# Optimization experiments

Hardware: AMD Instinct MI355X
Metric: run time of the kernel (lower is better)

The kernel has to match this reference:

```python
import jax, jax.numpy as jnp
import numpy as np

N_HEADS = 32
N_KV = 8
N_REP = N_HEADS // N_KV  # 4
HEAD_DIM = 128
DIM = 4096


def _rope(x, cos, sin, start_pos):
    # x: (B, H, T, hd); cos/sin: (max_seq, hd//2)
    T = x.shape[2]
    c = jax.lax.dynamic_slice_in_dim(cos, start_pos, T, axis=0)[None, None]  # (1,1,T,hd/2)
    s = jax.lax.dynamic_slice_in_dim(sin, start_pos, T, axis=0)[None, None]
    x1, x2 = x[..., : HEAD_DIM // 2], x[..., HEAD_DIM // 2:]
    return jnp.concatenate([x1 * c - x2 * s, x2 * c + x1 * s], axis=-1)


def setup_inputs() -> dict:
    key = jax.random.key(0)
    ks = jax.random.split(key, 7)
    B, T = 1, 2048
    sc = 0.02
    return {
        "x": jax.random.normal(ks[0], (B, T, DIM), jnp.float32),
        "cos": jax.random.normal(ks[1], (T, HEAD_DIM // 2), jnp.float32),
        "sin": jax.random.normal(ks[2], (T, HEAD_DIM // 2), jnp.float32),
        "wq": jax.random.normal(ks[3], (N_HEADS * HEAD_DIM, DIM), jnp.float32) * sc,
        "wk": jax.random.normal(ks[4], (N_KV * HEAD_DIM, DIM), jnp.float32) * sc,
        "wv": jax.random.normal(ks[5], (N_KV * HEAD_DIM, DIM), jnp.float32) * sc,
        "wo": jax.random.normal(ks[6], (DIM, DIM), jnp.float32) * sc,
        "start_pos": 0,
    }


def reference(x, cos, sin, wq, wk, wv, wo, start_pos):
    B, T, _ = x.shape
    # Projections (nn.Linear: y = x @ W^T)
    q = (x @ wq.T).reshape(B, T, N_HEADS, HEAD_DIM).transpose(0, 2, 1, 3)  # (B,Hq,T,hd)
    k = (x @ wk.T).reshape(B, T, N_KV, HEAD_DIM).transpose(0, 2, 1, 3)    # (B,Hk,T,hd)
    v = (x @ wv.T).reshape(B, T, N_KV, HEAD_DIM).transpose(0, 2, 1, 3)
    q = _rope(q, cos, sin, start_pos)
    k = _rope(k, cos, sin, start_pos)
    # GQA: group query heads per kv head instead of materializing repeat_kv
    qg = q.reshape(B, N_KV, N_REP, T, HEAD_DIM)
    scale = 1.0 / jnp.sqrt(jnp.float32(HEAD_DIM))
    scores = jnp.einsum('bgrqd,bgkd->bgrqk', qg, k) * scale  # (B,Hk,rep,T,T)
    causal = jnp.tril(jnp.ones((T, T), dtype=bool))
    scores = jnp.where(causal, scores, jnp.finfo(scores.dtype).min)
    attn = jax.nn.softmax(scores, axis=-1)
    yg = jnp.einsum('bgrqk,bgkd->bgrqd', attn, v)  # (B,Hk,rep,T,hd)
    y = yg.reshape(B, N_HEADS, T, HEAD_DIM).transpose(0, 2, 1, 3).reshape(B, T, DIM)
    return y @ wo.T
```

## Files before the change

kernel.cpp:

```cpp
#include <hip/hip_runtime.h>
#include <hip/hip_bf16.h>
#include <stdint.h>

using bf16 = __hip_bfloat16;
using bf16x8 = __attribute__((ext_vector_type(8))) short;
using f32x4  = __attribute__((ext_vector_type(4))) float;

#define AS1 __attribute__((address_space(1)))
#define AS3 __attribute__((address_space(3)))

__device__ __forceinline__ void async_ld16(const void* g, void* l) {
    __builtin_amdgcn_global_load_lds((const AS1 void*)g, (AS3 void*)l, 16, 0, 0);
}

__device__ __forceinline__ f32x4 mfma_bf16(bf16x8 a, bf16x8 b, f32x4 c) {
    return __builtin_amdgcn_mfma_f32_16x16x32_bf16(a, b, c, 0, 0, 0);
}

__device__ __forceinline__ float sexp(float x) {
    return __expf(fmaxf(x, -80.0f));
}

template<int N> __device__ __forceinline__ float dpp_max16(float x) {
    int xi = __builtin_bit_cast(int, x);
    int yi = __builtin_amdgcn_update_dpp(xi, xi, 0x110 | N, 0xf, 0xf, false);
    return fmaxf(x, __builtin_bit_cast(float, yi));
}
template<int N> __device__ __forceinline__ float dpp_add16(float x) {
    int xi = __builtin_bit_cast(int, x);
    int yi = __builtin_amdgcn_update_dpp(0, xi, 0x110 | N, 0xf, 0xf, true);
    return x + __builtin_bit_cast(float, yi);
}
__device__ __forceinline__ float bcast15(float x) {
    return __builtin_bit_cast(float,
        __builtin_amdgcn_ds_swizzle(__builtin_bit_cast(int, x), 0x01F0));
}
__device__ __forceinline__ float redmax16(float x) {
    x = dpp_max16<1>(x); x = dpp_max16<2>(x);
    x = dpp_max16<4>(x); x = dpp_max16<8>(x);
    return bcast15(x);
}
__device__ __forceinline__ float redsum16(float x) {
    x = dpp_add16<1>(x); x = dpp_add16<2>(x);
    x = dpp_add16<4>(x); x = dpp_add16<8>(x);
    return bcast15(x);
}

__device__ __forceinline__ void cvt8(const float* p, bf16* d) {
    float4 lo = *(const float4*)p;
    float4 hi = *(const float4*)(p + 4);
    bf16 t8[8] = {__float2bfloat16(lo.x), __float2bfloat16(lo.y),
                  __float2bfloat16(lo.z), __float2bfloat16(lo.w),
                  __float2bfloat16(hi.x), __float2bfloat16(hi.y),
                  __float2bfloat16(hi.z), __float2bfloat16(hi.w)};
    *(bf16x8*)d = *(const bf16x8*)t8;
}

__global__ __launch_bounds__(256) void cvt4_k(const float* __restrict__ x,  bf16* __restrict__ xb,
                                              const float* __restrict__ wq, bf16* __restrict__ wqb,
                                              const float* __restrict__ wk, bf16* __restrict__ wkb,
                                              const float* __restrict__ wv, bf16* __restrict__ wvb) {
    int stride = gridDim.x * blockDim.x;
    for (int u = blockIdx.x * blockDim.x + threadIdx.x; u < 4194304; u += stride) {
        const float* s; bf16* d; size_t off;
        if (u < 1048576)      { s = x;  d = xb;  off = (size_t)u * 8; }
        else if (u < 3145728) { s = wq; d = wqb; off = (size_t)(u - 1048576) * 8; }
        else if (u < 3670016) { s = wk; d = wkb; off = (size_t)(u - 3145728) * 8; }
        else                  { s = wv; d = wvb; off = (size_t)(u - 3670016) * 8; }
        cvt8(s + off, d + off);
    }
}

__global__ __launch_bounds__(256) void cvt_f32_bf16(const float* __restrict__ src,
                                                    bf16* __restrict__ dst, int n8) {
    int stride = gridDim.x * blockDim.x;
    for (int u = blockIdx.x * blockDim.x + threadIdx.x; u < n8; u += stride)
        cvt8(src + (size_t)u * 8, dst + (size_t)u * 8);
}

template<bool SRCF32>
__device__ __forceinline__ void stage_tile(const void* __restrict__ src,
                                           bf16* __restrict__ s,
                                           int row0, int K, int k0, int tid) {
    if constexpr (SRCF32) {
        const float* g = (const float*)src;
        #pragma unroll
        for (int i = 0; i < 2; ++i) {
            int u = tid + 256 * i;
            int row = u >> 2, c8 = (u & 3) * 8;
            cvt8(g + (size_t)(row0 + row) * K + k0 + c8, &s[row * 32 + c8]);
        }
    } else {
        const bf16* g = (const bf16*)src;
        const int wave = tid >> 6, lane = tid & 63;
        const int c0 = wave * 64 + lane;
        const int r0 = c0 >> 2, cb0 = (c0 & 3) * 16;
        const int c1 = 256 + c0;
        const int r1 = c1 >> 2, cb1 = (c1 & 3) * 16;
        async_ld16((const char*)(g + (size_t)(row0 + r0) * K + k0) + cb0,
                   (char*)s + wave * 1024);
        async_ld16((const char*)(g + (size_t)(row0 + r1) * K + k0) + cb1,
                   (char*)s + 4096 + wave * 1024);
    }
}

template<bool AF32, bool BF32, int MODE>
__global__ __launch_bounds__(256) void gemm_bt(const void* __restrict__ A,
                                               const void* __restrict__ B,
                                               void* __restrict__ C,
                                               bf16* __restrict__ Qp,
                                               bf16* __restrict__ Kp,
                                               bf16* __restrict__ Vp,
                                               int M, int N, int K) {
    __shared__ bf16 sA[128 * 32];
    __shared__ bf16 sB[128 * 32];
    const int tid  = threadIdx.x;
    const int lane = tid & 63;
    const int wave = tid >> 6;
    const int m0 = blockIdx.y * 128;
    const int n0 = blockIdx.x * 128;
    const int mrow = (wave >> 1) * 64;
    const int ncol = (wave & 1) * 64;

    f32x4 acc[4][4] = {};

    for (int k0 = 0; k0 < K; k0 += 32) {
        __syncthreads();
        stage_tile<AF32>(A, sA, m0, K, k0, tid);
        stage_tile<BF32>(B, sB, n0, K, k0, tid);
        __syncthreads();

        bf16x8 af[4], bfr[4];
        #pragma unroll
        for (int i = 0; i < 4; ++i)
            af[i] = *(const bf16x8*)&sA[(mrow + i * 16 + (lane & 15)) * 32 + (lane >> 4) * 8];
        #pragma unroll
        for (int j = 0; j < 4; ++j)
            bfr[j] = *(const bf16x8*)&sB[(ncol + j * 16 + (lane & 15)) * 32 + (lane >> 4) * 8];
        #pragma unroll
        for (int i = 0; i < 4; ++i)
            #pragma unroll
            for (int j = 0; j < 4; ++j)
                acc[i][j] = mfma_bf16(af[i], bfr[j], acc[i][j]);
    }

    #pragma unroll
    for (int i = 0; i < 4; ++i)
        #pragma unroll
        for (int j = 0; j < 4; ++j)
            #pragma unroll
            for (int r = 0; r < 4; ++r) {
                int row = m0 + mrow + i * 16 + (lane >> 4) * 4 + r;
                int col = n0 + ncol + j * 16 + (lane & 15);
                float fv = acc[i][j][r];
                if constexpr (MODE == 0) {
                    ((bf16*)C)[(size_t)row * N + col] = __float2bfloat16(fv);
                } else if constexpr (MODE == 1) {
                    ((bf16*)C)[(size_t)col * M + row] = __float2bfloat16(fv);
                } else if constexpr (MODE == 2) {
                    bf16 v = __float2bfloat16(fv);
                    if (col < 4096)      Qp[(size_t)row * 4096 + col] = v;
                    else if (col < 5120) Kp[(size_t)row * 1024 + (col - 4096)] = v;
                    else                 Vp[(size_t)(col - 5120) * 2048 + row] = v;
                } else {
                    ((float*)C)[(size_t)row * N + col] = fv;
                }
            }
}

#define VMW(N) asm volatile("s_waitcnt vmcnt(" #N ")" ::: "memory")
#define SCB    __builtin_amdgcn_sched_barrier(0)

#define TILE2(SA, SB, SA2, SB2, T2, DOST, WT) do {                                \
    bf16x8 aF0[4], bF0[4], aF1[4], bF1[4];                                        \
    _Pragma("unroll") for (int i = 0; i < 4; ++i)                                 \
        aF0[i] = *(const bf16x8*)((SA) + offA[i][0]);                             \
    _Pragma("unroll") for (int j = 0; j < 4; ++j)                                 \
        bF0[j] = *(const bf16x8*)((SB) + offB[j][0]);                             \
    SCB;                                                                          \
    _Pragma("unroll") for (int i = 0; i < 4; ++i)                                 \
        aF1[i] = *(const bf16x8*)((SA) + offA[i][1]);                             \
    _Pragma("unroll") for (int j = 0; j < 4; ++j)                                 \
        bF1[j] = *(const bf16x8*)((SB) + offB[j][1]);                             \
    SCB;                                                                          \
    if (DOST) { stgA01(SA2, T2); stgA23(SA2, T2); stgB0(SB2, T2); stgB1(SB2, T2); } \
    asm volatile("s_waitcnt lgkmcnt(8)" ::: "memory");                            \
    SCB;                                                                          \
    __builtin_amdgcn_s_setprio(1);                                                \
    _Pragma("unroll") for (int i = 0; i < 4; ++i)                                 \
      _Pragma("unroll") for (int j = 0; j < 4; ++j)                               \
        acc[i][j] = mfma_bf16(aF0[i], bF0[j], acc[i][j]);                         \
    __builtin_amdgcn_s_setprio(0);                                                \
    SCB;                                                                          \
    asm volatile("s_waitcnt lgkmcnt(0)" ::: "memory");                            \
    SCB;                                                                          \
    __builtin_amdgcn_s_setprio(1);                                                \
    _Pragma("unroll") for (int i = 0; i < 4; ++i)                                 \
      _Pragma("unroll") for (int j = 0; j < 4; ++j)                               \
        acc[i][j] = mfma_bf16(aF1[i], bF1[j], acc[i][j]);                         \
    __builtin_amdgcn_s_setprio(0);                                                \
    SCB;                                                                          \
    WT;                                                                           \
    __builtin_amdgcn_s_barrier();                                                 \
  } while (0)

template<int MODE>
__global__ __launch_bounds__(512, 1) void gemm_8p(const bf16* __restrict__ A,
                                                  const bf16* __restrict__ B,
                                                  void* __restrict__ C,
                                                  bf16* __restrict__ Qp,
                                                  bf16* __restrict__ Kp,
                                                  bf16* __restrict__ Vp,
                                                  int M, int N, int K) {
    __shared__ __align__(16) bf16 sA0[16384], sA1[16384], sA2[16384];
    __shared__ __align__(16) bf16 sB0[8192],  sB1[8192],  sB2[8192];

    const int tid  = threadIdx.x;
    const int lane = tid & 63;
    const int wave = tid >> 6;
    const int wr   = wave >> 1;
    const int wc   = wave & 1;
    const int m0 = blockIdx.y * 256;
    const int n0 = blockIdx.x * 128;
    const int NT = K >> 6;

    int offA[4][2], offB[4][2];
    {
        const int l15 = lane & 15, l4 = lane >> 4;
        #pragma unroll
        for (int i = 0; i < 4; ++i) {
            const int ra = wr * 64 + i * 16 + l15;
            const int rb = wc * 64 + i * 16 + l15;
            #pragma unroll
            for (int kh = 0; kh < 2; ++kh) {
                offA[i][kh] = ra * 64 + (((kh * 4 + l4) ^ (ra & 7)) * 8);
                offB[i][kh] = rb * 64 + (((kh * 4 + l4) ^ (rb & 7)) * 8);
            }
        }
    }

    const int rloc = tid >> 3;
    const int qsw  = (tid & 7) ^ (rloc & 7);
    const bf16* gA0 = A + (size_t)(m0 +   0 + rloc) * K + qsw * 8;
    const bf16* gA1 = A + (size_t)(m0 +  64 + rloc) * K + qsw * 8;
    const bf16* gA2 = A + (size_t)(m0 + 128 + rloc) * K + qsw * 8;
    const bf16* gA3 = A + (size_t)(m0 + 192 + rloc) * K + qsw * 8;
    const bf16* gB0 = B + (size_t)(n0 +   0 + rloc) * K + qsw * 8;
    const bf16* gB1 = B + (size_t)(n0 +  64 + rloc) * K + qsw * 8;
    const int w512 = wave * 512;

    auto stgA01 = [&](bf16* dst, int kt) __attribute__((always_inline)) {
        async_ld16(gA0 + kt * 64, dst + w512);
        async_ld16(gA1 + kt * 64, dst + 4096 + w512);
    };
    auto stgA23 = [&](bf16* dst, int kt) __attribute__((always_inline)) {
        async_ld16(gA2 + kt * 64, dst + 8192 + w512);
        async_ld16(gA3 + kt * 64, dst + 12288 + w512);
    };
    auto stgB0 = [&](bf16* dst, int kt) __attribute__((always_inline)) {
        async_ld16(gB0 + kt * 64, dst + w512);
    };
    auto stgB1 = [&](bf16* dst, int kt) __attribute__((always_inline)) {
        async_ld16(gB1 + kt * 64, dst + 4096 + w512);
    };

    f32x4 acc[4][4] = {};

    stgA01(sA0, 0); stgA23(sA0, 0); stgB0(sB0, 0); stgB1(sB0, 0);
    stgA01(sA1, 1); stgA23(sA1, 1); stgB0(sB1, 1); stgB1(sB1, 1);
    VMW(6);
    __builtin_amdgcn_s_barrier();
    asm volatile("" ::: "memory");
    SCB;

    int t = 0;
    for (; t < NT - 6; t += 3) {
        TILE2(sA0, sB0, sA2, sB2, t + 2, true, VMW(6));
        TILE2(sA1, sB1, sA0, sB0, t + 3, true, VMW(6));
        TILE2(sA2, sB2, sA1, sB1, t + 4, true, VMW(6));
    }
    TILE2(sA0, sB0, sA2, sB2, NT - 2, true,  VMW(6));
    TILE2(sA1, sB1, sA0, sB0, NT - 1, true,  VMW(6));
    TILE2(sA2, sB2, sA0, sB0, 0,      false, VMW(0));
    TILE2(sA0, sB0, sA1, sB1, 0,      false, );
    asm volatile("s_waitcnt vmcnt(0)" ::: "memory");

    #pragma unroll
    for (int i = 0; i < 4; ++i)
        #pragma unroll
        for (int j = 0; j < 4; ++j)
            #pragma unroll
            for (int r = 0; r < 4; ++r) {
                int row = m0 + wr * 64 + i * 16 + (lane >> 4) * 4 + r;
                int col = n0 + wc * 64 + j * 16 + (lane & 15);
                float fv = acc[i][j][r];
                if constexpr (MODE == 2) {
                    bf16 v = __float2bfloat16(fv);
                    if (col < 4096)      Qp[(size_t)row * 4096 + col] = v;
                    else if (col < 5120) Kp[(size_t)row * 1024 + (col - 4096)] = v;
                    else                 Vp[(size_t)(col - 5120) * 2048 + row] = v;
                } else {
                    ((float*)C)[(size_t)row * N + col] = fv;
                }
            }
}

__global__ __launch_bounds__(256) void rope_all(bf16* __restrict__ Q,
                                                bf16* __restrict__ K,
                                                const float* __restrict__ cosp,
                                                const float* __restrict__ sinp,
                                                const int* __restrict__ spp) {
    int idx = blockIdx.x * blockDim.x + threadIdx.x;
    int d = idx & 63;
    int h = (idx >> 6) % 40;
    int t = idx / (64 * 40);
    int sp = *spp;
    float c = cosp[(size_t)(t + sp) * 64 + d];
    float s = sinp[(size_t)(t + sp) * 64 + d];
    bf16* row = (h < 32) ? (Q + (size_t)t * 4096 + h * 128)
                         : (K + (size_t)t * 1024 + (h - 32) * 128);
    float x1 = __bfloat162float(row[d]);
    float x2 = __bfloat162float(row[64 + d]);
    row[d]      = __float2bfloat16(x1 * c - x2 * s);
    row[64 + d] = __float2bfloat16(x2 * c + x1 * s);
}

#define NEG_SENT (-1.0e9f)
__global__ __launch_bounds__(256) void attn_k(const bf16* __restrict__ Q,
                                              const bf16* __restrict__ K,
                                              const bf16* __restrict__ VT,
                                              bf16* __restrict__ Y) {
    constexpr int SKS = 136;
    constexpr int SVS = 72;
    __shared__ bf16 sK[64 * SKS];
    __shared__ bf16 sVT[128 * SVS];

    const int tid  = threadIdx.x;
    const int lane = tid & 63;
    const int wave = tid >> 6;
    const int qtile = 31 - (blockIdx.x >> 5);
    const int head  = blockIdx.x & 31;
    const int g     = head >> 2;
    const int qrow0 = qtile * 64 + wave * 16;
    bf16* sPw = sK + wave * 1152;

    bf16x8 qf[4];
    {
        const bf16* qbase = Q + (size_t)(qrow0 + (lane & 15)) * 4096 + head * 128;
        #pragma unroll
        for (int kk = 0; kk < 4; ++kk)
            qf[kk] = *(const bf16x8*)(qbase + kk * 32 + (lane >> 4) * 8);
    }

    float m_i[4], l_i[4];
    #pragma unroll
    for (int r = 0; r < 4; ++r) { m_i[r] = NEG_SENT; l_i[r] = 0.f; }
    f32x4 o[8] = {};
    const float scale = 0.08838834764831845f;

    for (int kt = 0; kt <= qtile; ++kt) {
        const int kt0 = kt * 64;
        __syncthreads();
        #pragma unroll
        for (int i = 0; i < 4; ++i) {
            int c = i * 256 + tid;
            {
                int row = c >> 4, ch = c & 15;
                *(uint4*)&sK[row * SKS + ch * 8] =
                    *(const uint4*)(K + (size_t)(kt0 + row) * 1024 + g * 128 + ch * 8);
            }
            {
                int row = c >> 3, ch = c & 7;
                *(uint4*)&sVT[row * SVS + ch * 8] =
                    *(const uint4*)(VT + (size_t)(g * 128 + row) * 2048 + kt0 + ch * 8);
            }
        }
        __syncthreads();

        f32x4 s[4];
        #pragma unroll
        for (int j = 0; j < 4; ++j) {
            f32x4 a = {};
            #pragma unroll
            for (int kk = 0; kk < 4; ++kk) {
                bf16x8 kfrag = *(const bf16x8*)&sK[(j * 16 + (lane & 15)) * SKS +
                                                   kk * 32 + (lane >> 4) * 8];
                a = mfma_bf16(qf[kk], kfrag, a);
            }
            s[j] = a;
        }

        #pragma unroll
        for (int j = 0; j < 4; ++j) {
            int tk = kt0 + j * 16 + (lane & 15);
            #pragma unroll
            for (int r = 0; r < 4; ++r) {
                int tq = qrow0 + (lane >> 4) * 4 + r;
                float v = s[j][r] * scale;
                s[j][r] = (tk > tq) ? NEG_SENT : v;
            }
        }

        #pragma unroll
        for (int r = 0; r < 4; ++r) {
            float mx = fmaxf(fmaxf(s[0][r], s[1][r]), fmaxf(s[2][r], s[3][r]));
            mx = redmax16(mx);
            float mn = fmaxf(m_i[r], mx);
            float alpha = sexp(m_i[r] - mn);
            m_i[r] = mn;
            float rs = 0.f;
            #pragma unroll
            for (int j = 0; j < 4; ++j) {
                float pv = sexp(s[j][r] - mn);
                s[j][r] = pv;
                rs += pv;
            }
            l_i[r] = l_i[r] * alpha + rs;
            #pragma unroll
            for (int j2 = 0; j2 < 8; ++j2) o[j2][r] *= alpha;
        }

        __syncthreads();

        #pragma unroll
        for (int j = 0; j < 4; ++j)
            #pragma unroll
            for (int r = 0; r < 4; ++r)
                sPw[((lane >> 4) * 4 + r) * SVS + j * 16 + (lane & 15)] =
                    __float2bfloat16(s[j][r]);
        __asm__ volatile("s_waitcnt lgkmcnt(0)" ::: "memory");

        #pragma unroll
        for (int kk2 = 0; kk2 < 2; ++kk2) {
            bf16x8 pf = *(const bf16x8*)&sPw[(lane & 15) * SVS + kk2 * 32 + (lane >> 4) * 8];
            #pragma unroll
            for (int j2 = 0; j2 < 8; ++j2) {
                bf16x8 vf = *(const bf16x8*)&sVT[(j2 * 16 + (lane & 15)) * SVS +
                                                 kk2 * 32 + (lane >> 4) * 8];
                o[j2] = mfma_bf16(pf, vf, o[j2]);
            }
        }
    }

    #pragma unroll
    for (int r = 0; r < 4; ++r) l_i[r] = redsum16(l_i[r]);
    #pragma unroll
    for (int j2 = 0; j2 < 8; ++j2)
        #pragma unroll
        for (int r = 0; r < 4; ++r) {
            int t   = qrow0 + (lane >> 4) * 4 + r;
            int col = head * 128 + j2 * 16 + (lane & 15);
            Y[(size_t)t * 4096 + col] = __float2bfloat16(o[j2][r] / l_i[r]);
        }
}

extern "C" void kernel_launch(void* const* d_in, const int* in_sizes, int n_in,
                              void* d_out, int out_size, void* d_ws, size_t ws_size,
                              hipStream_t stream) {
    const float* x    = (const float*)d_in[0];
    const float* cosp = (const float*)d_in[1];
    const float* sinp = (const float*)d_in[2];
    const float* wq   = (const float*)d_in[3];
    const float* wk   = (const float*)d_in[4];
    const float* wv   = (const float*)d_in[5];
    const float* wo   = (const float*)d_in[6];
    const int*   sp   = (const int*)d_in[7];
    float* out = (float*)d_out;

    char* ws = (char*)d_ws;
    bf16* Qb = (bf16*)d_out;

    const size_t NEED = 92274688;
    if (ws_size >= NEED) {
        bf16* xb   = (bf16*)(ws);
        bf16* wqkv = (bf16*)(ws + (16u << 20));
        bf16* wob  = wqkv;
        bf16* Kb   = (bf16*)(ws + (64u << 20));
        bf16* VT   = (bf16*)(ws + (68u << 20));
        bf16* Yb   = (bf16*)(ws + (72u << 20));

        cvt4_k<<<dim3(4096), 256, 0, stream>>>(x, xb, wq, wqkv,
                                               wk, wqkv + 16777216, wv, wqkv + 20971520);

        gemm_8p<2><<<dim3(48, 8), 512, 0, stream>>>(
            xb, wqkv, nullptr, Qb, Kb, VT, 2048, 6144, 4096);

        cvt_f32_bf16<<<dim3(4096), 256, 0, stream>>>(wo, wob, 2097152);

        rope_all<<<dim3(2048 * 40 * 64 / 256), 256, 0, stream>>>(Qb, Kb, cosp, sinp, sp);

        attn_k<<<dim3(1024), 256, 0, stream>>>(Qb, Kb, VT, Yb);

        gemm_8p<3><<<dim3(32, 8), 512, 0, stream>>>(
            Yb, wob, out, nullptr, nullptr, nullptr, 2048, 4096, 4096);
    } else {
        bf16* Kb = (bf16*)(ws);
        bf16* VT = (bf16*)(ws + (4u << 20));
        bf16* Yb = (bf16*)(ws + (8u << 20));

        gemm_bt<true, true, 0><<<dim3(32, 16), 256, 0, stream>>>(
            x, wq, Qb, nullptr, nullptr, nullptr, 2048, 4096, 4096);
        gemm_bt<true, true, 0><<<dim3(8, 16), 256, 0, stream>>>(
            x, wk, Kb, nullptr, nullptr, nullptr, 2048, 1024, 4096);
        gemm_bt<true, true, 1><<<dim3(8, 16), 256, 0, stream>>>(
            x, wv, VT, nullptr, nullptr, nullptr, 2048, 1024, 4096);

        rope_all<<<dim3(2048 * 40 * 64 / 256), 256, 0, stream>>>(Qb, Kb, cosp, sinp, sp);

        attn_k<<<dim3(1024), 256, 0, stream>>>(Qb, Kb, VT, Yb);

        gemm_bt<false, true, 3><<<dim3(32, 16), 256, 0, stream>>>(
            Yb, wo, out, nullptr, nullptr, nullptr, 2048, 4096, 4096);
    }
}
```

Before: 480.9 us.

## Templatize GEMM tile shape and give attention 32 query rows per wave

Makes the pipelined bf16 GEMM generic over block M, wave-column count and B fragments per wave. The QKV projection now uses a 128x192 tile on a 32x16 grid instead of 256x128 on 48x8, so more blocks cover the CUs. The attention kernel now processes 128 query rows per block, 32 per wave, so each K/V tile loaded to LDS feeds twice as many MFMAs, with a dedicated P buffer. This halves the attention grid and raises register pressure, and causal blocks now do more masked work on the diagonal.

```diff
diff --git a/kernel.cpp b/kernel.cpp
--- a/kernel.cpp
+++ b/kernel.cpp
@@ -45,6 +45,18 @@
     x = dpp_add16<4>(x); x = dpp_add16<8>(x);
     return bcast15(x);
 }
+
+template<int N> __device__ __forceinline__ void vmw() {
+    if constexpr (N == 0) asm volatile("s_waitcnt vmcnt(0)" ::: "memory");
+    else if constexpr (N == 5) asm volatile("s_waitcnt vmcnt(5)" ::: "memory");
+    else if constexpr (N == 6) asm volatile("s_waitcnt vmcnt(6)" ::: "memory");
+}
+template<int N> __device__ __forceinline__ void lgw() {
+    if constexpr (N == 0) asm volatile("s_waitcnt lgkmcnt(0)" ::: "memory");
+    else if constexpr (N == 7) asm volatile("s_waitcnt lgkmcnt(7)" ::: "memory");
+    else if constexpr (N == 8) asm volatile("s_waitcnt lgkmcnt(8)" ::: "memory");
+}
+#define SCB __builtin_amdgcn_sched_barrier(0)
 
 __device__ __forceinline__ void cvt8(const float* p, bf16* d) {
     float4 lo = *(const float4*)p;
@@ -168,131 +180,133 @@
             }
 }
 
-#define VMW(N) asm volatile("s_waitcnt vmcnt(" #N ")" ::: "memory")
-#define SCB    __builtin_amdgcn_sched_barrier(0)
-
-#define TILE2(SA, SB, SA2, SB2, T2, DOST, WT) do {                                \
-    bf16x8 aF0[4], bF0[4], aF1[4], bF1[4];                                        \
+#define KTILE(SA, SB, SA2, SB2, T2, DOST, WTN) do {                               \
+    bf16x8 aF0[4], bF0[NFr], aF1[4], bF1[NFr];                                    \
     _Pragma("unroll") for (int i = 0; i < 4; ++i)                                 \
         aF0[i] = *(const bf16x8*)((SA) + offA[i][0]);                             \
-    _Pragma("unroll") for (int j = 0; j < 4; ++j)                                 \
+    _Pragma("unroll") for (int j = 0; j < NFr; ++j)                               \
         bF0[j] = *(const bf16x8*)((SB) + offB[j][0]);                             \
     SCB;                                                                          \
     _Pragma("unroll") for (int i = 0; i < 4; ++i)                                 \
         aF1[i] = *(const bf16x8*)((SA) + offA[i][1]);                             \
-    _Pragma("unroll") for (int j = 0; j < 4; ++j)                                 \
+    _Pragma("unroll") for (int j = 0; j < NFr; ++j)                               \
         bF1[j] = *(const bf16x8*)((SB) + offB[j][1]);                             \
     SCB;                                                                          \
-    if (DOST) { stgA01(SA2, T2); stgA23(SA2, T2); stgB0(SB2, T2); stgB1(SB2, T2); } \
-    asm volatile("s_waitcnt lgkmcnt(8)" ::: "memory");                            \
+    if (DOST) { stgA(SA2, T2); stgB(SB2, T2); }                                   \
+    lgw<4 + NFr>();                                                               \
     SCB;                                                                          \
     __builtin_amdgcn_s_setprio(1);                                                \
     _Pragma("unroll") for (int i = 0; i < 4; ++i)                                 \
-      _Pragma("unroll") for (int j = 0; j < 4; ++j)                               \
+      _Pragma("unroll") for (int j = 0; j < NFr; ++j)                             \
         acc[i][j] = mfma_bf16(aF0[i], bF0[j], acc[i][j]);                         \
     __builtin_amdgcn_s_setprio(0);                                                \
     SCB;                                                                          \
-    asm volatile("s_waitcnt lgkmcnt(0)" ::: "memory");                            \
+    lgw<0>();                                                                     \
     SCB;                                                                          \
     __builtin_amdgcn_s_setprio(1);                                                \
     _Pragma("unroll") for (int i = 0; i < 4; ++i)                                 \
-      _Pragma("unroll") for (int j = 0; j < 4; ++j)                               \
+      _Pragma("unroll") for (int j = 0; j < NFr; ++j)                             \
         acc[i][j] = mfma_bf16(aF1[i], bF1[j], acc[i][j]);                         \
     __builtin_amdgcn_s_setprio(0);                                                \
     SCB;                                                                          \
-    WT;                                                                           \
+    vmw<WTN>();                                                                   \
     __builtin_amdgcn_s_barrier();                                                 \
   } while (0)
 
-template<int MODE>
-__global__ __launch_bounds__(512, 1) void gemm_8p(const bf16* __restrict__ A,
+template<int MODE, int BM, int NWC, int NFr>
+__global__ __launch_bounds__(512, 1) void gemm_kt(const bf16* __restrict__ A,
                                                   const bf16* __restrict__ B,
                                                   void* __restrict__ C,
                                                   bf16* __restrict__ Qp,
                                                   bf16* __restrict__ Kp,
                                                   bf16* __restrict__ Vp,
                                                   int M, int N, int K) {
-    __shared__ __align__(16) bf16 sA0[16384], sA1[16384], sA2[16384];
-    __shared__ __align__(16) bf16 sB0[8192],  sB1[8192],  sB2[8192];
+    constexpr int BN  = NWC * NFr * 16;
+    constexpr int IA  = BM / 64;
+    constexpr int IB  = BN / 64;
+    constexpr int IPT = IA + IB;
+
+    __shared__ __align__(16) bf16 sA0[BM * 64], sA1[BM * 64], sA2[BM * 64];
+    __shared__ __align__(16) bf16 sB0[BN * 64], sB1[BN * 64], sB2[BN * 64];
 
     const int tid  = threadIdx.x;
     const int lane = tid & 63;
     const int wave = tid >> 6;
-    const int wr   = wave >> 1;
-    const int wc   = wave & 1;
-    const int m0 = blockIdx.y * 256;
-    const int n0 = blockIdx.x * 128;
+    const int wr   = wave / NWC;
+    const int wc   = wave % NWC;
+    const int m0 = blockIdx.y * BM;
+    const int n0 = blockIdx.x * BN;
     const int NT = K >> 6;
 
-    int offA[4][2], offB[4][2];
+    int offA[4][2], offB[NFr][2];
     {
         const int l15 = lane & 15, l4 = lane >> 4;
         #pragma unroll
         for (int i = 0; i < 4; ++i) {
             const int ra = wr * 64 + i * 16 + l15;
-            const int rb = wc * 64 + i * 16 + l15;
-            #pragma unroll
-            for (int kh = 0; kh < 2; ++kh) {
+            #pragma unroll
+            for (int kh = 0; kh < 2; ++kh)
                 offA[i][kh] = ra * 64 + (((kh * 4 + l4) ^ (ra & 7)) * 8);
-                offB[i][kh] = rb * 64 + (((kh * 4 + l4) ^ (rb & 7)) * 8);
-            }
+        }
+        #pragma unroll
+        for (int j = 0; j < NFr; ++j) {
+            const int rb = wc * (NFr * 16) + j * 16 + l15;
+            #pragma unroll
+            for (int kh = 0; kh < 2; ++kh)
+                offB[j][kh] = rb * 64 + (((kh * 4 + l4) ^ (rb & 7)) * 8);
         }
     }
 
     const int rloc = tid >> 3;
     const int qsw  = (tid & 7) ^ (rloc & 7);
-    const bf16* gA0 = A + (size_t)(m0 +   0 + rloc) * K + qsw * 8;
-    const bf16* gA1 = A + (size_t)(m0 +  64 + rloc) * K + qsw * 8;
-    const bf16* gA2 = A + (size_t)(m0 + 128 + rloc) * K + qsw * 8;
-    const bf16* gA3 = A + (size_t)(m0 + 192 + rloc) * K + qsw * 8;
-    const bf16* gB0 = B + (size_t)(n0 +   0 + rloc) * K + qsw * 8;
-    const bf16* gB1 = B + (size_t)(n0 +  64 + rloc) * K + qsw * 8;
+    const bf16* gA[IA];
+    const bf16* gB[IB];
+    #pragma unroll
+    for (int k = 0; k < IA; ++k) gA[k] = A + (size_t)(m0 + k * 64 + rloc) * K + qsw * 8;
+    #pragma unroll
+    for (int k = 0; k < IB; ++k) gB[k] = B + (size_t)(n0 + k * 64 + rloc) * K + qsw * 8;
     const int w512 = wave * 512;
 
-    auto stgA01 = [&](bf16* dst, int kt) __attribute__((always_inline)) {
-        async_ld16(gA0 + kt * 64, dst + w512);
-        async_ld16(gA1 + kt * 64, dst + 4096 + w512);
+    auto stgA = [&](bf16* dst, int kt) __attribute__((always_inline)) {
+        #pragma unroll
+        for (int k = 0; k < IA; ++k)
+            async_ld16(gA[k] + kt * 64, dst + k * 4096 + w512);
     };
-    auto stgA23 = [&](bf16* dst, int kt) __attribute__((always_inline)) {
-        async_ld16(gA2 + kt * 64, dst + 8192 + w512);
-        async_ld16(gA3 + kt * 64, dst + 12288 + w512);
+    auto stgB = [&](bf16* dst, int kt) __attribute__((always_inline)) {
+        #pragma unroll
+        for (int k = 0; k < IB; ++k)
+            async_ld16(gB[k] + kt * 64, dst + k * 4096 + w512);
     };
-    auto stgB0 = [&](bf16* dst, int kt) __attribute__((always_inline)) {
-        async_ld16(gB0 + kt * 64, dst + w512);
-    };
-    auto stgB1 = [&](bf16* dst, int kt) __attribute__((always_inline)) {
-        async_ld16(gB1 + kt * 64, dst + 4096 + w512);
-    };
-
-    f32x4 acc[4][4] = {};
-
-    stgA01(sA0, 0); stgA23(sA0, 0); stgB0(sB0, 0); stgB1(sB0, 0);
-    stgA01(sA1, 1); stgA23(sA1, 1); stgB0(sB1, 1); stgB1(sB1, 1);
-    VMW(6);
+
+    f32x4 acc[4][NFr] = {};
+
+    stgA(sA0, 0); stgB(sB0, 0);
+    stgA(sA1, 1); stgB(sB1, 1);
+    vmw<IPT>();
     __builtin_amdgcn_s_barrier();
     asm volatile("" ::: "memory");
     SCB;
 
     int t = 0;
     for (; t < NT - 6; t += 3) {
-        TILE2(sA0, sB0, sA2, sB2, t + 2, true, VMW(6));
-        TILE2(sA1, sB1, sA0, sB0, t + 3, true, VMW(6));
-        TILE2(sA2, sB2, sA1, sB1, t + 4, true, VMW(6));
-    }
-    TILE2(sA0, sB0, sA2, sB2, NT - 2, true,  VMW(6));
-    TILE2(sA1, sB1, sA0, sB0, NT - 1, true,  VMW(6));
-    TILE2(sA2, sB2, sA0, sB0, 0,      false, VMW(0));
-    TILE2(sA0, sB0, sA1, sB1, 0,      false, );
+        KTILE(sA0, sB0, sA2, sB2, t + 2, true, IPT);
+        KTILE(sA1, sB1, sA0, sB0, t + 3, true, IPT);
+        KTILE(sA2, sB2, sA1, sB1, t + 4, true, IPT);
+    }
+    KTILE(sA0, sB0, sA2, sB2, NT - 2, true,  IPT);
+    KTILE(sA1, sB1, sA0, sB0, NT - 1, true,  IPT);
+    KTILE(sA2, sB2, sA0, sB0, 0,      false, 0);
+    KTILE(sA0, sB0, sA1, sB1, 0,      false, -1);
     asm volatile("s_waitcnt vmcnt(0)" ::: "memory");
 
     #pragma unroll
     for (int i = 0; i < 4; ++i)
         #pragma unroll
-        for (int j = 0; j < 4; ++j)
+        for (int j = 0; j < NFr; ++j)
             #pragma unroll
             for (int r = 0; r < 4; ++r) {
                 int row = m0 + wr * 64 + i * 16 + (lane >> 4) * 4 + r;
-                int col = n0 + wc * 64 + j * 16 + (lane & 15);
+                int col = n0 + wc * (NFr * 16) + j * 16 + (lane & 15);
                 float fv = acc[i][j][r];
                 if constexpr (MODE == 2) {
                     bf16 v = __float2bfloat16(fv);
@@ -326,39 +340,44 @@
 }
 
 #define NEG_SENT (-1.0e9f)
-__global__ __launch_bounds__(256) void attn_k(const bf16* __restrict__ Q,
-                                              const bf16* __restrict__ K,
-                                              const bf16* __restrict__ VT,
-                                              bf16* __restrict__ Y) {
+__global__ __launch_bounds__(256) void attn_k2(const bf16* __restrict__ Q,
+                                               const bf16* __restrict__ K,
+                                               const bf16* __restrict__ VT,
+                                               bf16* __restrict__ Y) {
     constexpr int SKS = 136;
     constexpr int SVS = 72;
     __shared__ bf16 sK[64 * SKS];
     __shared__ bf16 sVT[128 * SVS];
+    __shared__ bf16 sP[128 * SVS];
 
     const int tid  = threadIdx.x;
     const int lane = tid & 63;
     const int wave = tid >> 6;
-    const int qtile = 31 - (blockIdx.x >> 5);
+    const int qtile = 15 - (blockIdx.x >> 5);
     const int head  = blockIdx.x & 31;
     const int g     = head >> 2;
-    const int qrow0 = qtile * 64 + wave * 16;
-    bf16* sPw = sK + wave * 1152;
-
-    bf16x8 qf[4];
-    {
-        const bf16* qbase = Q + (size_t)(qrow0 + (lane & 15)) * 4096 + head * 128;
+    const int qrow0 = qtile * 128 + wave * 32;
+    bf16* sPw = sP + wave * 32 * SVS;
+
+    bf16x8 qf[2][4];
+    #pragma unroll
+    for (int mi = 0; mi < 2; ++mi) {
+        const bf16* qbase = Q + (size_t)(qrow0 + mi * 16 + (lane & 15)) * 4096 + head * 128;
         #pragma unroll
         for (int kk = 0; kk < 4; ++kk)
-            qf[kk] = *(const bf16x8*)(qbase + kk * 32 + (lane >> 4) * 8);
-    }
-
-    float m_i[4], l_i[4];
-    #pragma unroll
-    for (int r = 0; r < 4; ++r) { m_i[r] = NEG_SENT; l_i[r] = 0.f; }
-    f32x4 o[8] = {};
+            qf[mi][kk] = *(const bf16x8*)(qbase + kk * 32 + (lane >> 4) * 8);
+    }
+
+    float m_i[2][4], l_i[2][4];
+    #pragma unroll
+    for (int mi = 0; mi < 2; ++mi)
+        #pragma unroll
+        for (int r = 0; r < 4; ++r) { m_i[mi][r] = NEG_SENT; l_i[mi][r] = 0.f; }
+    f32x4 o[2][8] = {};
     const float scale = 0.08838834764831845f;
 
-    for (int kt = 0; kt <= qtile; ++kt) {
+    const int ktn = 2 * qtile + 2;
+    for (int kt = 0; kt < ktn; ++kt) {
         const int kt0 = kt * 64;
         __syncthreads();
         #pragma unroll
@@ -377,81 +396,98 @@
         }
         __syncthreads();
 
-        f32x4 s[4];
-        #pragma unroll
-        for (int j = 0; j < 4; ++j) {
-            f32x4 a = {};
-            #pragma unroll
-            for (int kk = 0; kk < 4; ++kk) {
-                bf16x8 kfrag = *(const bf16x8*)&sK[(j * 16 + (lane & 15)) * SKS +
-                                                   kk * 32 + (lane >> 4) * 8];
-                a = mfma_bf16(qf[kk], kfrag, a);
-            }
-            s[j] = a;
-        }
-
-        #pragma unroll
-        for (int j = 0; j < 4; ++j) {
-            int tk = kt0 + j * 16 + (lane & 15);
+        f32x4 s[2][4];
+        #pragma unroll
+        for (int mi = 0; mi < 2; ++mi)
+            #pragma unroll
+            for (int j = 0; j < 4; ++j) {
+                f32x4 a = {};
+                #pragma unroll
+                for (int kk = 0; kk < 4; ++kk) {
+                    bf16x8 kfrag = *(const bf16x8*)&sK[(j * 16 + (lane & 15)) * SKS +
+                                                       kk * 32 + (lane >> 4) * 8];
+                    a = mfma_bf16(qf[mi][kk], kfrag, a);
+                }
+                s[mi][j] = a;
+            }
+
+        #pragma unroll
+        for (int mi = 0; mi < 2; ++mi)
+            #pragma unroll
+            for (int j = 0; j < 4; ++j) {
+                int tk = kt0 + j * 16 + (lane & 15);
+                #pragma unroll
+                for (int r = 0; r < 4; ++r) {
+                    int tq = qrow0 + mi * 16 + (lane >> 4) * 4 + r;
+                    float v = s[mi][j][r] * scale;
+                    s[mi][j][r] = (tk > tq) ? NEG_SENT : v;
+                }
+            }
+
+        #pragma unroll
+        for (int mi = 0; mi < 2; ++mi)
             #pragma unroll
             for (int r = 0; r < 4; ++r) {
-                int tq = qrow0 + (lane >> 4) * 4 + r;
-                float v = s[j][r] * scale;
-                s[j][r] = (tk > tq) ? NEG_SENT : v;
-            }
-        }
-
-        #pragma unroll
-        for (int r = 0; r < 4; ++r) {
-            float mx = fmaxf(fmaxf(s[0][r], s[1][r]), fmaxf(s[2][r], s[3][r]));
-            mx = redmax16(mx);
-            float mn = fmaxf(m_i[r], mx);
-            float alpha = sexp(m_i[r] - mn);
-            m_i[r] = mn;
-            float rs = 0.f;
-            #pragma unroll
-            for (int j = 0; j < 4; ++j) {
-                float pv = sexp(s[j][r] - mn);
-                s[j][r] = pv;
-                rs += pv;
-            }
-            l_i[r] = l_i[r] * alpha + rs;
-            #pragma unroll
-            for (int j2 = 0; j2 < 8; ++j2) o[j2][r] *= alpha;
-        }
-
-        __syncthreads();
-
-        #pragma unroll
-        for (int j = 0; j < 4; ++j)
-            #pragma unroll
-            for (int r = 0; r < 4; ++r)
-                sPw[((lane >> 4) * 4 + r) * SVS + j * 16 + (lane & 15)] =
-                    __float2bfloat16(s[j][r]);
+                float mx = fmaxf(fmaxf(s[mi][0][r], s[mi][1][r]),
+                                 fmaxf(s[mi][2][r], s[mi][3][r]));
+                mx = redmax16(mx);
+                float mn = fmaxf(m_i[mi][r], mx);
+                float alpha = sexp(m_i[mi][r] - mn);
+                m_i[mi][r] = mn;
+                float rs = 0.f;
+                #pragma unroll
+                for (int j = 0; j < 4; ++j) {
+                    float pv = sexp(s[mi][j][r] - mn);
+                    s[mi][j][r] = pv;
+                    rs += pv;
+                }
+                l_i[mi][r] = l_i[mi][r] * alpha + rs;
+                #pragma unroll
+                for (int j2 = 0; j2 < 8; ++j2) o[mi][j2][r] *= alpha;
+            }
+
+        #pragma unroll
+        for (int mi = 0; mi < 2; ++mi)
+            #pragma unroll
+            for (int j = 0; j < 4; ++j)
+                #pragma unroll
+                for (int r = 0; r < 4; ++r)
+                    sPw[(mi * 16 + (lane >> 4) * 4 + r) * SVS + j * 16 + (lane & 15)] =
+                        __float2bfloat16(s[mi][j][r]);
         __asm__ volatile("s_waitcnt lgkmcnt(0)" ::: "memory");
 
         #pragma unroll
         for (int kk2 = 0; kk2 < 2; ++kk2) {
-            bf16x8 pf = *(const bf16x8*)&sPw[(lane & 15) * SVS + kk2 * 32 + (lane >> 4) * 8];
+            bf16x8 pf[2];
+            #pragma unroll
+            for (int mi = 0; mi < 2; ++mi)
+                pf[mi] = *(const bf16x8*)&sPw[(mi * 16 + (lane & 15)) * SVS +
+                                              kk2 * 32 + (lane >> 4) * 8];
             #pragma unroll
             for (int j2 = 0; j2 < 8; ++j2) {
                 bf16x8 vf = *(const bf16x8*)&sVT[(j2 * 16 + (lane & 15)) * SVS +
                                                  kk2 * 32 + (lane >> 4) * 8];
-                o[j2] = mfma_bf16(pf, vf, o[j2]);
+                #pragma unroll
+                for (int mi = 0; mi < 2; ++mi)
+                    o[mi][j2] = mfma_bf16(pf[mi], vf, o[mi][j2]);
             }
         }
     }
 
     #pragma unroll
-    for (int r = 0; r < 4; ++r) l_i[r] = redsum16(l_i[r]);
-    #pragma unroll
-    for (int j2 = 0; j2 < 8; ++j2)
-        #pragma unroll
-        for (int r = 0; r < 4; ++r) {
-            int t   = qrow0 + (lane >> 4) * 4 + r;
-            int col = head * 128 + j2 * 16 + (lane & 15);
-            Y[(size_t)t * 4096 + col] = __float2bfloat16(o[j2][r] / l_i[r]);
-        }
+    for (int mi = 0; mi < 2; ++mi)
+        #pragma unroll
+        for (int r = 0; r < 4; ++r) l_i[mi][r] = redsum16(l_i[mi][r]);
+    #pragma unroll
+    for (int mi = 0; mi < 2; ++mi)
+        #pragma unroll
+        for (int j2 = 0; j2 < 8; ++j2)
+            #pragma unroll
+            for (int r = 0; r < 4; ++r) {
+                int t   = qrow0 + mi * 16 + (lane >> 4) * 4 + r;
+                int col = head * 128 + j2 * 16 + (lane & 15);
+                Y[(size_t)t * 4096 + col] = __float2bfloat16(o[mi][j2][r] / l_i[mi][r]);
+            }
 }
 
 extern "C" void kernel_launch(void* const* d_in, const int* in_sizes, int n_in,
@@ -482,16 +518,16 @@
         cvt4_k<<<dim3(4096), 256, 0, stream>>>(x, xb, wq, wqkv,
                                                wk, wqkv + 16777216, wv, wqkv + 20971520);
 
-        gemm_8p<2><<<dim3(48, 8), 512, 0, stream>>>(
+        gemm_kt<2, 128, 4, 3><<<dim3(32, 16), 512, 0, stream>>>(
             xb, wqkv, nullptr, Qb, Kb, VT, 2048, 6144, 4096);
 
         cvt_f32_bf16<<<dim3(4096), 256, 0, stream>>>(wo, wob, 2097152);
 
         rope_all<<<dim3(2048 * 40 * 64 / 256), 256, 0, stream>>>(Qb, Kb, cosp, sinp, sp);
 
-        attn_k<<<dim3(1024), 256, 0, stream>>>(Qb, Kb, VT, Yb);
-
-        gemm_8p<3><<<dim3(32, 8), 512, 0, stream>>>(
+        attn_k2<<<dim3(512), 256, 0, stream>>>(Qb, Kb, VT, Yb);
+
+        gemm_kt<3, 256, 2, 4><<<dim3(32, 8), 512, 0, stream>>>(
             Yb, wob, out, nullptr, nullptr, nullptr, 2048, 4096, 4096);
     } else {
         bf16* Kb = (bf16*)(ws);
@@ -507,7 +543,7 @@
 
         rope_all<<<dim3(2048 * 40 * 64 / 256), 256, 0, stream>>>(Qb, Kb, cosp, sinp, sp);
 
-        attn_k<<<dim3(1024), 256, 0, stream>>>(Qb, Kb, VT, Yb);
+        attn_k2<<<dim3(512), 256, 0, stream>>>(Qb, Kb, VT, Yb);
 
         gemm_bt<false, true, 3><<<dim3(32, 16), 256, 0, stream>>>(
             Yb, wo, out, nullptr, nullptr, nullptr, 2048, 4096, 4096);
```

Measured after the change: 499.7 us. +3.9%, slower.
